# Kernel optimization log

Measured on AMD Instinct MI355X. Metric: run time of the kernel, lower is better.

Reference implementation:

```python
import jax, jax.numpy as jnp
import numpy as np

M_USERS = 100000
N_ITEMS = 50000
N_NODES = M_USERS + N_ITEMS
DIM = 64
N_INTER = 1600000
BATCH = 16384
N_NEG = 40
REG = 1e-4


def setup_inputs() -> dict:
    key = jax.random.key(0)
    ks = jax.random.split(key, 12)
    xavier = lambda k, shape: jax.random.normal(k, shape, jnp.float32) * np.sqrt(2.0 / (shape[-1] + shape[-2] if len(shape) >= 2 else shape[-1] + 1))
    E = jax.random.normal(ks[0], (N_NODES, DIM), jnp.float32) * 0.1
    E2 = jax.random.normal(ks[1], (N_NODES, DIM), jnp.float32) * 0.1
    Wm = jax.random.normal(ks[2], (2, DIM, DIM), jnp.float32) * np.sqrt(1.0 / DIM)
    bm = jnp.zeros((2, DIM), jnp.float32)
    attn_W = jax.random.normal(ks[3], (DIM, DIM), jnp.float32) * np.sqrt(1.0 / DIM)
    attn_b = jnp.zeros((DIM,), jnp.float32)
    q_w = jax.random.normal(ks[4], (DIM,), jnp.float32) * np.sqrt(1.0 / DIM)
    # symmetric bipartite edge list: users in [0, M), items in [M, M+N)
    eu = jax.random.randint(ks[5], (N_INTER,), 0, M_USERS, jnp.int32)
    ei = jax.random.randint(ks[6], (N_INTER,), M_USERS, N_NODES, jnp.int32)
    edge_index = jnp.stack([jnp.concatenate([eu, ei]), jnp.concatenate([ei, eu])], axis=0)
    u = jax.random.randint(ks[7], (BATCH,), 0, M_USERS, jnp.int32)
    v = jax.random.randint(ks[8], (BATCH,), M_USERS, N_NODES, jnp.int32)
    n = jax.random.randint(ks[9], (BATCH, N_NEG), M_USERS, N_NODES, jnp.int32)
    w = jax.random.uniform(ks[10], (BATCH,), jnp.float32, 0.5, 5.0)  # ratings; only sign() used
    return {"E": E, "E2": E2, "Wm": Wm, "bm": bm, "attn_W": attn_W, "attn_b": attn_b,
            "q_w": q_w, "edge_index": edge_index, "u": u, "v": v, "n": n, "w": w}


def _lightgconv(x, src, dst, norm):
    # out[i] = sum_{(j->i)} norm_e * x[j]   (symmetric-normalized LightGCN propagate)
    msg = x[src] * norm[:, None]  # [E, D]
    return jax.ops.segment_sum(msg, dst, num_segments=N_NODES)


def _aggregate(E, E2, Wm, bm, attn_W, attn_b, q_w, edge_index):
    src, dst = edge_index[0], edge_index[1]
    deg = jax.ops.segment_sum(jnp.ones(src.shape, E.dtype), dst, num_segments=N_NODES)
    dinv = jnp.where(deg > 0, jax.lax.rsqrt(jnp.maximum(deg, 1.0)), 0.0)
    norm = dinv[src] * dinv[dst]
    # GNN branch: B = [E, conv(E), conv(conv(E))]; z_p = mean
    b1 = _lightgconv(E, src, dst, norm)
    b2 = _lightgconv(b1, src, dst, norm)
    z_p = (E + b1 + b2) / 3.0
    # MLP branch (eval mode: dropout disabled); z_n is output of last MLP layer
    x = jax.nn.relu(E2 @ Wm[0].T + bm[0])
    x = jax.nn.relu(x @ Wm[1].T + bm[1])
    z_n = x
    # attention fusion
    w_p = jnp.tanh(z_p @ attn_W.T + attn_b) @ q_w  # [Nn]
    w_n = jnp.tanh(z_n @ attn_W.T + attn_b) @ q_w  # [Nn]
    alpha = jax.nn.softmax(jnp.stack([w_p, w_n], axis=1), axis=1)  # [Nn, 2]
    return alpha[:, 0:1] * z_p + alpha[:, 1:2] * z_n


def reference(E, E2, Wm, bm, attn_W, attn_b, q_w, edge_index, u, v, n, w):
    Z = _aggregate(E, E2, Wm, bm, attn_W, attn_b, q_w, edge_index)
    u_ = Z[u]            # [B, D]
    v_ = Z[v]            # [B, D]
    n_ = Z[n]            # [B, K, D]
    pos = jnp.sum(u_ * v_, axis=1)                      # [B]
    neg = jnp.einsum('bd,bkd->bk', u_, n_)              # [B, K]
    sbpr = jax.nn.log_sigmoid(jnp.sign(w)[:, None] * pos[:, None] - neg).sum(axis=1)
    reg_loss = jnp.sum(u_ ** 2) + jnp.sum(v_ ** 2) + jnp.sum(n_ ** 2)
    return -jnp.sum(sbpr) + REG * reg_loss
```

## Files before the change

kernel.cpp:

```cpp
#include <hip/hip_runtime.h>
#include <math.h>


typedef unsigned int uint;
typedef unsigned short ushort;
typedef unsigned long long ull;
typedef __attribute__((ext_vector_type(8))) short short8v;
typedef __attribute__((ext_vector_type(4))) float float4v;
typedef __attribute__((ext_vector_type(2))) float float2v;

#define BK_SHIFT 9
#define BK_SIZE 512
#define CAP 20480
#define SRC_BITS 18
#define SRC_MASK ((1u << SRC_BITS) - 1u)

#if __has_builtin(__builtin_amdgcn_cvt_pk_f32_fp8) && __has_builtin(__builtin_amdgcn_cvt_pk_fp8_f32)
#define HW_FP8 1
#else
#define HW_FP8 0
#endif

__device__ inline float b2f(ushort u) { return __uint_as_float(((uint)u) << 16); }
__device__ inline ushort f2b(float f) {
  uint u = __float_as_uint(f);
  return (ushort)((u + 0x7fffu + ((u >> 16) & 1u)) >> 16);
}
__device__ inline uint pack2(float lo, float hi) {
  return (uint)f2b(lo) | ((uint)f2b(hi) << 16);
}

__device__ inline float dec1(uint u) {
  uint e = (u >> 3) & 0xFu;
  uint m = u & 7u;
  uint s = (u & 0x80u) << 24;
  float norm = __uint_as_float(s | ((e + 120u) << 23) | (m << 20));
  float den = __uint_as_float(s | 0x3F800000u) * (float)(int)m * 0.001953125f;
  return e ? norm : den;
}
__device__ inline uint enc1(float x) {
  uint s = (__float_as_uint(x) >> 24) & 0x80u;
  float ax = fminf(fabsf(x), 448.f);
  uint r;
  if (ax < 0.015625f) {
    r = (uint)(int)rintf(ax * 512.f);
  } else {
    uint b = __float_as_uint(ax);
    b += 0x7FFFFu + ((b >> 20) & 1u);
    uint e = (b >> 23) - 120u;
    r = (e > 15u) ? 0x7Eu : ((e << 3) | ((b >> 20) & 7u));
  }
  return s | r;
}
__device__ inline float4 dec4(uint v) {
#if HW_FP8
  float2v lo = __builtin_amdgcn_cvt_pk_f32_fp8((int)v, false);
  float2v hi = __builtin_amdgcn_cvt_pk_f32_fp8((int)v, true);
  return make_float4(lo[0], lo[1], hi[0], hi[1]);
#else
  return make_float4(dec1(v & 0xFFu), dec1((v >> 8) & 0xFFu),
                     dec1((v >> 16) & 0xFFu), dec1(v >> 24));
#endif
}
__device__ inline uint enc4f(float a, float b, float c, float d) {
#if HW_FP8
  int v = 0;
  v = __builtin_amdgcn_cvt_pk_fp8_f32(a, b, v, false);
  v = __builtin_amdgcn_cvt_pk_fp8_f32(c, d, v, true);
  return (uint)v;
#else
  return enc1(a) | (enc1(b) << 8) | (enc1(c) << 16) | (enc1(d) << 24);
#endif
}

__global__ void k_conv(const float* __restrict__ E, const float* __restrict__ E2,
                       const float* __restrict__ dinv,
                       uint* __restrict__ E8s, ushort* __restrict__ Ebf,
                       ushort* __restrict__ E2h, int n4) {
  int i = blockIdx.x * blockDim.x + threadIdx.x;
  if (i >= n4) return;
  int node = i >> 2;
  float dn = dinv[node];
  const float4* pe = (const float4*)(E + (size_t)i * 16);
  float4 f0 = pe[0], f1 = pe[1], f2 = pe[2], f3 = pe[3];
  uint4 o8;
  o8.x = enc4f(dn * f0.x, dn * f0.y, dn * f0.z, dn * f0.w);
  o8.y = enc4f(dn * f1.x, dn * f1.y, dn * f1.z, dn * f1.w);
  o8.z = enc4f(dn * f2.x, dn * f2.y, dn * f2.z, dn * f2.w);
  o8.w = enc4f(dn * f3.x, dn * f3.y, dn * f3.z, dn * f3.w);
  ((uint4*)E8s)[i] = o8;
  uint4 h0, h1;
  h0.x = pack2(f0.x, f0.y); h0.y = pack2(f0.z, f0.w);
  h0.z = pack2(f1.x, f1.y); h0.w = pack2(f1.z, f1.w);
  h1.x = pack2(f2.x, f2.y); h1.y = pack2(f2.z, f2.w);
  h1.z = pack2(f3.x, f3.y); h1.w = pack2(f3.z, f3.w);
  ((uint4*)Ebf)[2 * i] = h0;
  ((uint4*)Ebf)[2 * i + 1] = h1;
  const float4* p2 = (const float4*)(E2 + (size_t)i * 16);
  float4 g0 = p2[0], g1 = p2[1], g2 = p2[2], g3 = p2[3];
  uint4 e0, e1;
  e0.x = pack2(g0.x, g0.y); e0.y = pack2(g0.z, g0.w);
  e0.z = pack2(g1.x, g1.y); e0.w = pack2(g1.z, g1.w);
  e1.x = pack2(g2.x, g2.y); e1.y = pack2(g2.z, g2.w);
  e1.z = pack2(g3.x, g3.y); e1.w = pack2(g3.z, g3.w);
  ((uint4*)E2h)[2 * i] = e0;
  ((uint4*)E2h)[2 * i + 1] = e1;
}

__global__ void k_convw(const float* __restrict__ Wm, const float* __restrict__ AW,
                        ushort* __restrict__ Wmh, ushort* __restrict__ AWh) {
  int i = blockIdx.x * blockDim.x + threadIdx.x;
  const float* srcp;
  ushort* dstp;
  if (i < 1024) { srcp = Wm + (size_t)i * 8; dstp = Wmh + (size_t)i * 8; }
  else if (i < 1536) { srcp = AW + (size_t)(i - 1024) * 8; dstp = AWh + (size_t)(i - 1024) * 8; }
  else return;
  float4 a = ((const float4*)srcp)[0], b = ((const float4*)srcp)[1];
  uint4 o;
  o.x = pack2(a.x, a.y); o.y = pack2(a.z, a.w);
  o.z = pack2(b.x, b.y); o.w = pack2(b.z, b.w);
  *(uint4*)dstp = o;
}

__global__ __launch_bounds__(512) void k_bucket(const int* __restrict__ src,
                                                const int* __restrict__ dst,
                                                int* __restrict__ gcursor,
                                                uint* __restrict__ ebuf,
                                                int NE, int nbkt, int chunk) {
  __shared__ int hist[1024];
  __shared__ int curb[1024];
  int tid = threadIdx.x;
  int nt = blockDim.x;
  for (int g = tid; g < nbkt; g += nt) hist[g] = 0;
  __syncthreads();
  int lo = blockIdx.x * chunk;
  int hi = min(lo + chunk, NE);
  for (int e = lo + tid; e < hi; e += nt)
    atomicAdd(&hist[dst[e] >> BK_SHIFT], 1);
  __syncthreads();
  for (int g = tid; g < nbkt; g += nt) {
    int c = hist[g];
    curb[g] = (c > 0) ? atomicAdd(&gcursor[g], c) : 0;
  }
  __syncthreads();
  for (int e = lo + tid; e < hi; e += nt) {
    int d = dst[e];
    int g = d >> BK_SHIFT;
    int pos = atomicAdd(&curb[g], 1);
    if (pos < CAP)
      ebuf[(size_t)g * CAP + pos] = ((uint)(d & (BK_SIZE - 1)) << SRC_BITS) | (uint)src[e];
  }
}

__global__ void k_small(const int* __restrict__ gcursor, int* __restrict__ bktbase,
                        int nbkt) {
  __shared__ int sm[1024];
  int t = threadIdx.x;
  int v = (t < nbkt) ? gcursor[t] : 0;
  sm[t] = v;
  __syncthreads();
  for (int off = 1; off < 1024; off <<= 1) {
    int a = (t >= off) ? sm[t - off] : 0;
    __syncthreads();
    sm[t] += a;
    __syncthreads();
  }
  if (t < nbkt) bktbase[t] = sm[t] - v;
  if (t == 0) bktbase[nbkt] = sm[1023];
}

__global__ __launch_bounds__(256) void k_fine(const uint* __restrict__ ebuf,
                                              const int* __restrict__ gcursor,
                                              const int* __restrict__ bktbase,
                                              int* __restrict__ rowptr,
                                              float* __restrict__ dinv,
                                              int* __restrict__ csrc,
                                              int NN, int nbkt) {
  __shared__ int degl[BK_SIZE];
  __shared__ int lpl[BK_SIZE];
  __shared__ int ssum[256];
  int g = blockIdx.x;
  int tid = threadIdx.x;
  int cnt = gcursor[g];
  int base = bktbase[g];
  size_t ebase = (size_t)g * CAP;
  for (int j = tid; j < BK_SIZE; j += 256) degl[j] = 0;
  __syncthreads();
  for (int i = tid; i < cnt; i += 256)
    atomicAdd(&degl[(int)(ebuf[ebase + i] >> SRC_BITS)], 1);
  __syncthreads();
  int d0 = degl[2 * tid], d1 = degl[2 * tid + 1];
  int s = d0 + d1;
  ssum[tid] = s;
  __syncthreads();
  for (int off = 1; off < 256; off <<= 1) {
    int a = (tid >= off) ? ssum[tid - off] : 0;
    __syncthreads();
    ssum[tid] += a;
    __syncthreads();
  }
  int excl = ssum[tid] - s;
  lpl[2 * tid] = excl;
  lpl[2 * tid + 1] = excl + d0;
  int node0 = g * BK_SIZE;
  int n0 = node0 + 2 * tid, n1 = n0 + 1;
  if (n0 < NN) {
    rowptr[n0] = base + excl;
    dinv[n0] = (d0 > 0) ? rsqrtf((float)d0) : 0.f;
  }
  if (n1 < NN) {
    rowptr[n1] = base + excl + d0;
    dinv[n1] = (d1 > 0) ? rsqrtf((float)d1) : 0.f;
  }
  if (g == nbkt - 1 && tid == 255) rowptr[NN] = base + excl + d0 + d1;
  __syncthreads();
  for (int i = tid; i < cnt; i += 256) {
    uint e = ebuf[ebase + i];
    int dl = (int)(e >> SRC_BITS);
    int r = atomicAdd(&lpl[dl], 1);
    csrc[base + r] = (int)(e & SRC_MASK);
  }
}

__global__ __launch_bounds__(256) void k_gather(const uint* __restrict__ x,
                                                const int* __restrict__ rowptr,
                                                const int* __restrict__ csrc,
                                                const float* __restrict__ dinv,
                                                uint* __restrict__ out1,
                                                uint* __restrict__ outs, int NN) {
  int gid = blockIdx.x * blockDim.x + threadIdx.x;
  int node = gid >> 4;
  if (node >= NN) return;
  int sl = gid & 15;
  int beg = rowptr[node], end = rowptr[node + 1];
  float dn = dinv[node];
  float a0 = 0.f, a1 = 0.f, a2 = 0.f, a3 = 0.f;
  int i = beg;
  for (; i + 3 < end; i += 4) {
    int s0 = csrc[i], s1 = csrc[i + 1], s2 = csrc[i + 2], s3 = csrc[i + 3];
    uint r0 = x[(size_t)s0 * 16 + sl];
    uint r1 = x[(size_t)s1 * 16 + sl];
    uint r2 = x[(size_t)s2 * 16 + sl];
    uint r3 = x[(size_t)s3 * 16 + sl];
    float4 d0 = dec4(r0), d1 = dec4(r1), d2 = dec4(r2), d3 = dec4(r3);
    a0 += d0.x + d1.x + d2.x + d3.x;
    a1 += d0.y + d1.y + d2.y + d3.y;
    a2 += d0.z + d1.z + d2.z + d3.z;
    a3 += d0.w + d1.w + d2.w + d3.w;
  }
  for (; i < end; ++i) {
    float4 d0 = dec4(x[(size_t)csrc[i] * 16 + sl]);
    a0 += d0.x; a1 += d0.y; a2 += d0.z; a3 += d0.w;
  }
  out1[(size_t)node * 16 + sl] = enc4f(a0 * dn, a1 * dn, a2 * dn, a3 * dn);
  if (outs) {
    float dn2 = dn * dn;
    outs[(size_t)node * 16 + sl] = enc4f(a0 * dn2, a1 * dn2, a2 * dn2, a3 * dn2);
  }
}

__device__ inline float fast_tanh(float x) {
  float t = __expf(fminf(fmaxf(2.f * x, -30.f), 30.f));
  return (t - 1.f) / (t + 1.f);
}

#define MFMA(a, b, c) __builtin_amdgcn_mfma_f32_16x16x32_bf16((a), (b), (c), 0, 0, 0)

__global__ __launch_bounds__(256, 2) void k_node(const ushort* __restrict__ Ebf,
                                                 const ushort* __restrict__ E2h,
                                                 const ushort* __restrict__ Wmh,
                                                 const float* __restrict__ bm,
                                                 const ushort* __restrict__ AWh,
                                                 const float* __restrict__ ab,
                                                 const float* __restrict__ qw,
                                                 const uint* __restrict__ b1q,
                                                 const uint* __restrict__ b2q,
                                                 uint* __restrict__ Z8,
                                                 int NN) {
  __shared__ ushort Hl[64 * 72];
  __shared__ ushort Pl[64 * 72];
  int tid = threadIdx.x;
  int lane = tid & 63, wid = tid >> 6;
  int r15 = lane & 15, kg = lane >> 4;
  int node0 = blockIdx.x * 64;

  int arow = node0 + 16 * wid + r15;
  int arowc = min(arow, NN - 1);
  const ushort* e2p = E2h + (size_t)arowc * 64 + 8 * kg;
  short8v a0 = *(const short8v*)e2p;
  short8v a1 = *(const short8v*)(e2p + 32);
  float4v acc[4];
#pragma unroll
  for (int b = 0; b < 4; ++b) {
    int col = r15 + 16 * b;
    short8v w0 = *(const short8v*)&Wmh[col * 64 + 8 * kg];
    short8v w1 = *(const short8v*)&Wmh[col * 64 + 32 + 8 * kg];
    float bias = bm[col];
    acc[b] = (float4v){bias, bias, bias, bias};
    acc[b] = MFMA(a0, w0, acc[b]);
    acc[b] = MFMA(a1, w1, acc[b]);
  }
#pragma unroll
  for (int b = 0; b < 4; ++b)
#pragma unroll
    for (int rr = 0; rr < 4; ++rr)
      Hl[(16 * wid + 4 * kg + rr) * 72 + 16 * b + r15] = f2b(fmaxf(acc[b][rr], 0.f));

  {
    int row = tid >> 2;
    int c4 = (tid & 3) * 4;
    int node = node0 + row;
    uint outp[8];
    if (node < NN) {
      const ushort* pe = Ebf + (size_t)node * 64 + c4 * 4;
      uint4 eh0 = *(const uint4*)pe;
      uint4 eh1 = *(const uint4*)(pe + 8);
      uint4 q1 = *(const uint4*)(b1q + (size_t)node * 16 + c4);
      uint4 q2 = *(const uint4*)(b2q + (size_t)node * 16 + c4);
      float4 d1[4] = {dec4(q1.x), dec4(q1.y), dec4(q1.z), dec4(q1.w)};
      float4 d2[4] = {dec4(q2.x), dec4(q2.y), dec4(q2.z), dec4(q2.w)};
      uint ehall[8] = {eh0.x, eh0.y, eh0.z, eh0.w, eh1.x, eh1.y, eh1.z, eh1.w};
#pragma unroll
      for (int c = 0; c < 4; ++c) {
        float e0 = b2f((ushort)(ehall[2 * c] & 0xFFFFu));
        float e1 = b2f((ushort)(ehall[2 * c] >> 16));
        float e2 = b2f((ushort)(ehall[2 * c + 1] & 0xFFFFu));
        float e3 = b2f((ushort)(ehall[2 * c + 1] >> 16));
        float z0 = (e0 + d1[c].x + d2[c].x) * (1.f / 3.f);
        float z1 = (e1 + d1[c].y + d2[c].y) * (1.f / 3.f);
        float z2 = (e2 + d1[c].z + d2[c].z) * (1.f / 3.f);
        float z3 = (e3 + d1[c].w + d2[c].w) * (1.f / 3.f);
        outp[2 * c] = pack2(z0, z1);
        outp[2 * c + 1] = pack2(z2, z3);
      }
    } else {
#pragma unroll
      for (int c = 0; c < 8; ++c) outp[c] = 0;
    }
    int c0 = c4 * 4;
    *(uint4*)&Pl[row * 72 + c0] = *(uint4*)&outp[0];
    *(uint4*)&Pl[row * 72 + c0 + 8] = *(uint4*)&outp[4];
  }
  __syncthreads();

  const ushort* hap = &Hl[(16 * wid + r15) * 72 + 8 * kg];
  short8v ha0 = *(const short8v*)hap;
  short8v ha1 = *(const short8v*)(hap + 32);
  float4v acc2[4];
#pragma unroll
  for (int b = 0; b < 4; ++b) {
    int col = r15 + 16 * b;
    short8v w0 = *(const short8v*)&Wmh[4096 + col * 64 + 8 * kg];
    short8v w1 = *(const short8v*)&Wmh[4096 + col * 64 + 32 + 8 * kg];
    float bias = bm[64 + col];
    acc2[b] = (float4v){bias, bias, bias, bias};
    acc2[b] = MFMA(ha0, w0, acc2[b]);
    acc2[b] = MFMA(ha1, w1, acc2[b]);
  }
  __syncthreads();
#pragma unroll
  for (int b = 0; b < 4; ++b)
#pragma unroll
    for (int rr = 0; rr < 4; ++rr)
      Hl[(16 * wid + 4 * kg + rr) * 72 + 16 * b + r15] = f2b(fmaxf(acc2[b][rr], 0.f));
  __syncthreads();

  const ushort* pap = &Pl[(16 * wid + r15) * 72 + 8 * kg];
  short8v pa0 = *(const short8v*)pap;
  short8v pa1 = *(const short8v*)(pap + 32);
  const ushort* nap = &Hl[(16 * wid + r15) * 72 + 8 * kg];
  short8v na0 = *(const short8v*)nap;
  short8v na1 = *(const short8v*)(nap + 32);
  float4v ac1[4], ac2[4];
#pragma unroll
  for (int b = 0; b < 4; ++b) {
    int col = r15 + 16 * b;
    short8v w0 = *(const short8v*)&AWh[col * 64 + 8 * kg];
    short8v w1 = *(const short8v*)&AWh[col * 64 + 32 + 8 * kg];
    float bias = ab[col];
    ac1[b] = (float4v){bias, bias, bias, bias};
    ac1[b] = MFMA(pa0, w0, ac1[b]);
    ac1[b] = MFMA(pa1, w1, ac1[b]);
    ac2[b] = (float4v){bias, bias, bias, bias};
    ac2[b] = MFMA(na0, w0, ac2[b]);
    ac2[b] = MFMA(na1, w1, ac2[b]);
  }

  float qv[4];
#pragma unroll
  for (int b = 0; b < 4; ++b) qv[b] = qw[r15 + 16 * b];
#pragma unroll
  for (int rr = 0; rr < 4; ++rr) {
    float wp = 0.f, wn = 0.f;
#pragma unroll
    for (int b = 0; b < 4; ++b) {
      wp += fast_tanh(ac1[b][rr]) * qv[b];
      wn += fast_tanh(ac2[b][rr]) * qv[b];
    }
#pragma unroll
    for (int off = 8; off; off >>= 1) {
      wp += __shfl_xor(wp, off);
      wn += __shfl_xor(wn, off);
    }
    float m = fmaxf(wp, wn);
    float e1 = __expf(wp - m), e2 = __expf(wn - m);
    float inv = 1.f / (e1 + e2);
    float al0 = e1 * inv, al1 = e2 * inv;
    int row_l = 16 * wid + 4 * kg + rr;
#pragma unroll
    for (int b = 0; b < 4; ++b) {
      int li = row_l * 72 + r15 + 16 * b;
      Pl[li] = f2b(al0 * b2f(Pl[li]) + al1 * b2f(Hl[li]));
    }
  }
  __syncthreads();

  {
    int row = tid >> 2;
    int c0 = (tid & 3) * 16;
    int node = node0 + row;
    if (node < NN) {
      const ushort* zp = &Pl[row * 72 + c0];
      uint4 o;
      o.x = enc4f(b2f(zp[0]), b2f(zp[1]), b2f(zp[2]), b2f(zp[3]));
      o.y = enc4f(b2f(zp[4]), b2f(zp[5]), b2f(zp[6]), b2f(zp[7]));
      o.z = enc4f(b2f(zp[8]), b2f(zp[9]), b2f(zp[10]), b2f(zp[11]));
      o.w = enc4f(b2f(zp[12]), b2f(zp[13]), b2f(zp[14]), b2f(zp[15]));
      *(uint4*)&Z8[(size_t)node * 16 + (tid & 3) * 4] = o;
    }
  }
}

__global__ __launch_bounds__(256) void k_score(const uint* __restrict__ Z,
                                               const int* __restrict__ u,
                                               const int* __restrict__ v,
                                               const int* __restrict__ n,
                                               const float* __restrict__ w,
                                               float* __restrict__ out, int B, int K) {
  __shared__ float xbuf[16][44];
  __shared__ float part[16];
  int t = threadIdx.x;
  int wv = t >> 6, lane = t & 63;
  int sg = lane >> 4, sl = lane & 15;
  int bloc = wv * 4 + sg;
  int b = blockIdx.x * 16 + bloc;
  float lossb = 0.f;
  if (b < B) {
    int uid = u[b], vid = v[b];
    float4 u4 = dec4(Z[(size_t)uid * 16 + sl]);
    float4 v4 = dec4(Z[(size_t)vid * 16 + sl]);
    float p = u4.x * v4.x + u4.y * v4.y + u4.z * v4.z + u4.w * v4.w;
#pragma unroll
    for (int off = 8; off; off >>= 1) p += __shfl_xor(p, off);
    float wb = w[b];
    float sgn = (wb > 0.f) ? 1.f : ((wb < 0.f) ? -1.f : 0.f);
    float sp = sgn * p;
    float regl = u4.x * u4.x + u4.y * u4.y + u4.z * u4.z + u4.w * u4.w
               + v4.x * v4.x + v4.y * v4.y + v4.z * v4.z + v4.w * v4.w;
    const int* nb_ = n + (size_t)b * K;
    for (int k = 0; k < K; ++k) {
      int nid = nb_[k];
      float4 n4 = dec4(Z[(size_t)nid * 16 + sl]);
      float d = u4.x * n4.x + u4.y * n4.y + u4.z * n4.z + u4.w * n4.w;
      regl += n4.x * n4.x + n4.y * n4.y + n4.z * n4.z + n4.w * n4.w;
#pragma unroll
      for (int off = 8; off; off >>= 1) d += __shfl_xor(d, off);
      if (sl == 0) xbuf[bloc][k] = sp - d;
    }
#pragma unroll
    for (int off = 8; off; off >>= 1) regl += __shfl_xor(regl, off);
    float sb = 0.f;
    for (int k = sl; k < K; k += 16) {
      float x = xbuf[bloc][k];
      sb += fminf(x, 0.f) - log1pf(__expf(-fabsf(x)));
    }
#pragma unroll
    for (int off = 8; off; off >>= 1) sb += __shfl_xor(sb, off);
    lossb = -sb + 1e-4f * regl;
  }
  if (sl == 0) part[bloc] = (b < B) ? lossb : 0.f;
  __syncthreads();
  if (t == 0) {
    float s = 0.f;
#pragma unroll
    for (int i = 0; i < 16; ++i) s += part[i];
    unsafeAtomicAdd(out, s);
  }
}

extern "C" void kernel_launch(void* const* d_in, const int* in_sizes, int n_in,
                              void* d_out, int out_size, void* d_ws, size_t ws_size,
                              hipStream_t stream) {
  const float* E  = (const float*)d_in[0];
  const float* E2 = (const float*)d_in[1];
  const float* Wm = (const float*)d_in[2];
  const float* bm = (const float*)d_in[3];
  const float* AW = (const float*)d_in[4];
  const float* ab = (const float*)d_in[5];
  const float* qw = (const float*)d_in[6];
  const int*   ei = (const int*)d_in[7];
  const int*   u  = (const int*)d_in[8];
  const int*   v  = (const int*)d_in[9];
  const int*   nn = (const int*)d_in[10];
  const float* w  = (const float*)d_in[11];

  const int NN = in_sizes[0] / 64;
  const int NE = in_sizes[7] / 2;
  const int B  = in_sizes[8];
  const int K  = in_sizes[10] / B;
  const int NBKT = (NN + BK_SIZE - 1) / BK_SIZE;

  const int* src = ei;
  const int* dst = ei + NE;

  float*  ws      = (float*)d_ws;
  float*  dinv    = ws;
  uint*   E8s     = (uint*)(dinv + NN);
  uint*   b1q     = E8s + (size_t)NN * 16;
  uint*   b1s     = b1q + (size_t)NN * 16;
  uint*   b2q     = b1s + (size_t)NN * 16;
  ushort* E2h     = (ushort*)(b2q + (size_t)NN * 16);
  ushort* Wmh     = E2h + (size_t)NN * 64;
  ushort* AWh     = Wmh + 8192;
  int*    rowptr  = (int*)(AWh + 4096);
  int*    csrc    = rowptr + NN + 1;
  int*    gcursor = csrc + NE;
  int*    bktbase = gcursor + NBKT;
  uint*   ebuf    = (uint*)(((uintptr_t)(bktbase + NBKT + 1) + 15) & ~(uintptr_t)15);
  uint*   Z8      = ebuf;
  ushort* Ebf     = (ushort*)(Z8 + (size_t)NN * 16);
  float*  outf    = (float*)d_out;

  hipMemsetAsync(gcursor, 0, (size_t)NBKT * sizeof(int), stream);
  hipMemsetAsync(outf, 0, sizeof(float), stream);

  const int BUCKET_BLOCKS = 512;
  int chunk = (NE + BUCKET_BLOCKS - 1) / BUCKET_BLOCKS;
  k_bucket<<<BUCKET_BLOCKS, 512, 0, stream>>>(src, dst, gcursor, ebuf, NE, NBKT, chunk);
  k_small<<<1, 1024, 0, stream>>>(gcursor, bktbase, NBKT);
  k_fine<<<NBKT, 256, 0, stream>>>(ebuf, gcursor, bktbase, rowptr, dinv, csrc, NN, NBKT);

  k_conv<<<(NN * 4 + 255) / 256, 256, 0, stream>>>(E, E2, dinv, E8s, Ebf, E2h, NN * 4);
  k_convw<<<6, 256, 0, stream>>>(Wm, AW, Wmh, AWh);

  int gatherBlocks = ((size_t)NN * 16 + 255) / 256;
  k_gather<<<gatherBlocks, 256, 0, stream>>>(E8s, rowptr, csrc, dinv, b1q, b1s, NN);
  k_gather<<<gatherBlocks, 256, 0, stream>>>(b1s, rowptr, csrc, dinv, b2q, (uint*)nullptr, NN);

  int nodeTiles = (NN + 63) / 64;
  k_node<<<nodeTiles, 256, 0, stream>>>(Ebf, E2h, Wmh, bm, AWh, ab, qw, b1q, b2q, Z8, NN);

  k_score<<<(B + 15) / 16, 256, 0, stream>>>(Z8, u, v, nn, w, outf, B, K);
}
```

Measured before the change: 273.9 us.

## Stage bucketed edges in LDS and write them to global memory contiguously

The edge-bucketing kernel now sorts each block's chunk by bucket in shared memory. It builds a local prefix scan of the per-bucket counts, scatters the packed edges into an LDS staging buffer, and then writes them out linearly. Each thread binary-searches the local offsets to find the global destination. The aim is to turn fully random 4-byte global writes into contiguous runs per bucket, which coalesce better. In exchange it adds a block-wide scan, an extra barrier phase and LDS pressure, and it relies on the number of buckets fitting in 512 and the chunk size fitting in CHUNK_MAX.

```diff
diff --git a/kernel.cpp b/kernel.cpp
--- a/kernel.cpp
+++ b/kernel.cpp
@@ -14,6 +14,7 @@
 #define CAP 20480
 #define SRC_BITS 18
 #define SRC_MASK ((1u << SRC_BITS) - 1u)
+#define CHUNK_MAX 6272
 
 #if __has_builtin(__builtin_amdgcn_cvt_pk_f32_fp8) && __has_builtin(__builtin_amdgcn_cvt_pk_fp8_f32)
 #define HW_FP8 1
@@ -127,28 +128,54 @@
                                                 int* __restrict__ gcursor,
                                                 uint* __restrict__ ebuf,
                                                 int NE, int nbkt, int chunk) {
-  __shared__ int hist[1024];
-  __shared__ int curb[1024];
+  __shared__ uint stage[CHUNK_MAX];
+  __shared__ int hist[512];
+  __shared__ int lbase[513];
+  __shared__ int gbase[512];
+  __shared__ int sm[512];
   int tid = threadIdx.x;
   int nt = blockDim.x;
-  for (int g = tid; g < nbkt; g += nt) hist[g] = 0;
+  for (int g = tid; g < 512; g += nt) hist[g] = 0;
   __syncthreads();
   int lo = blockIdx.x * chunk;
   int hi = min(lo + chunk, NE);
   for (int e = lo + tid; e < hi; e += nt)
     atomicAdd(&hist[dst[e] >> BK_SHIFT], 1);
   __syncthreads();
-  for (int g = tid; g < nbkt; g += nt) {
-    int c = hist[g];
-    curb[g] = (c > 0) ? atomicAdd(&gcursor[g], c) : 0;
+  int v = (tid < nbkt) ? hist[tid] : 0;
+  sm[tid] = v;
+  __syncthreads();
+  for (int off = 1; off < 512; off <<= 1) {
+    int a = (tid >= off) ? sm[tid - off] : 0;
+    __syncthreads();
+    sm[tid] += a;
+    __syncthreads();
+  }
+  if (tid < nbkt) lbase[tid] = sm[tid] - v;
+  if (tid == 0) lbase[nbkt] = sm[511];
+  if (tid < nbkt) {
+    gbase[tid] = (v > 0) ? atomicAdd(&gcursor[tid], v) : 0;
+    hist[tid] = 0;
   }
   __syncthreads();
   for (int e = lo + tid; e < hi; e += nt) {
     int d = dst[e];
     int g = d >> BK_SHIFT;
-    int pos = atomicAdd(&curb[g], 1);
-    if (pos < CAP)
-      ebuf[(size_t)g * CAP + pos] = ((uint)(d & (BK_SIZE - 1)) << SRC_BITS) | (uint)src[e];
+    int pos = atomicAdd(&hist[g], 1);
+    stage[lbase[g] + pos] = ((uint)(d & (BK_SIZE - 1)) << SRC_BITS) | (uint)src[e];
+  }
+  __syncthreads();
+  int total = lbase[nbkt];
+  for (int i = tid; i < total; i += nt) {
+    int loI = 0, hiI = nbkt;
+    while (hiI - loI > 1) {
+      int mid = (loI + hiI) >> 1;
+      if (lbase[mid] <= i) loI = mid; else hiI = mid;
+    }
+    int g = loI;
+    int off = gbase[g] + (i - lbase[g]);
+    if (off < CAP)
+      ebuf[(size_t)g * CAP + off] = stage[i];
   }
 }
 
```

Result: no change. 278.1 us (+1.5%).
